# Performance work log

Hardware: AMD Instinct MI355X
Metric: run time of the kernel (lower is better)

The kernel has to match this reference:

```python
import jax, jax.numpy as jnp
import numpy as np

IMG = 640.0
BOX_W, OBJ_W, CLS_W = 7.5, 1.0, 0.5
EPS = 1e-7


def bce_logits(x, t):
    # numerically stable BCE-with-logits, reduction='none'
    return jnp.maximum(x, 0.0) - x * t + jnp.log1p(jnp.exp(-jnp.abs(x)))


def cxcywh_to_xyxy(b):
    cx, cy, w, h = b[..., 0], b[..., 1], b[..., 2], b[..., 3]
    return jnp.stack([cx - w / 2, cy - h / 2, cx + w / 2, cy + h / 2], axis=-1)


def ciou_elementwise(p, g):
    # p, g: (N,4) xyxy; returns CIoU per pair (diag of pairwise matrix)
    px1, py1, px2, py2 = p[:, 0], p[:, 1], p[:, 2], p[:, 3]
    gx1, gy1, gx2, gy2 = g[:, 0], g[:, 1], g[:, 2], g[:, 3]
    iw = jnp.clip(jnp.minimum(px2, gx2) - jnp.maximum(px1, gx1), 0.0)
    ih = jnp.clip(jnp.minimum(py2, gy2) - jnp.maximum(py1, gy1), 0.0)
    inter = iw * ih
    union = (px2 - px1) * (py2 - py1) + (gx2 - gx1) * (gy2 - gy1) - inter
    iou = inter / (union + EPS)
    cw = jnp.maximum(px2, gx2) - jnp.minimum(px1, gx1)
    ch = jnp.maximum(py2, gy2) - jnp.minimum(py1, gy1)
    c2 = cw * cw + ch * ch + EPS
    rho2 = ((gx1 + gx2 - px1 - px2) ** 2 + (gy1 + gy2 - py1 - py2) ** 2) / 4.0
    wp, hp = px2 - px1, py2 - py1
    wg, hg = gx2 - gx1, gy2 - gy1
    v = (4.0 / (jnp.pi ** 2)) * (jnp.arctan(wg / (hg + EPS)) - jnp.arctan(wp / (hp + EPS))) ** 2
    alpha = v / (1.0 - iou + v + EPS)
    return iou - rho2 / c2 - alpha * v


def _per_image(decoded, obj_map, cls_map, boxes, labels, min_sz, max_sz):
    # decoded (4,H,W) normalized cxcywh; obj_map (H,W); cls_map (C,H,W)
    C, H, W = cls_map.shape
    tmax = jnp.maximum(boxes[:, 2], boxes[:, 3]) * IMG
    mask = (tmax > min_sz) & (tmax <= max_sz)        # (N,)
    m = mask.astype(decoded.dtype)
    gx = jnp.clip((boxes[:, 0] * W).astype(jnp.int32), 0, W - 1)
    gy = jnp.clip((boxes[:, 1] * H).astype(jnp.int32), 0, H - 1)
    mp_box = decoded[:, gy, gx].T                    # (N,4)
    iou = jnp.clip(ciou_elementwise(cxcywh_to_xyxy(mp_box), cxcywh_to_xyxy(boxes)), -1.0, 1.0)
    box_l = jnp.sum((1.0 - iou) * m)
    mp_cls = cls_map[:, gy, gx].T                    # (N,C)
    onehot = jax.nn.one_hot(labels, C, dtype=cls_map.dtype)
    cls_l = jnp.sum(bce_logits(mp_cls, onehot) * m[:, None])
    mp_obj = obj_map[gy, gx]
    obj_pos = jnp.sum(bce_logits(mp_obj, 1.0) * m)
    # negative mask: 0 at cells hit by a valid GT, 1 elsewhere
    mask_neg = jnp.ones((H, W), obj_map.dtype).at[gy, gx].min(jnp.where(mask, 0.0, 1.0))
    neg_map = bce_logits(obj_map, 0.0)
    obj_neg = jnp.sum(neg_map * mask_neg) * 0.05
    fallback = jnp.mean(neg_map) * 0.1               # no positives at this scale for this image
    has_pos = jnp.sum(mask) > 0
    obj_l = jnp.where(has_pos, obj_pos + obj_neg, fallback)
    return jnp.where(has_pos, box_l, 0.0), obj_l, jnp.where(has_pos, cls_l, 0.0), jnp.sum(mask)


def detection_loss(p3_bbox, p3_obj, p3_cls, p4_bbox, p4_obj, p4_cls,
                   p5_bbox, p5_obj, p5_cls, boxes, labels):
    B = p3_bbox.shape[0]
    scales = [(p3_bbox, p3_obj, p3_cls, 8, 0.0, 64.0),
              (p4_bbox, p4_obj, p4_cls, 16, 64.0, 128.0),
              (p5_bbox, p5_obj, p5_cls, 32, 128.0, 10000.0)]
    tot_box = tot_obj = tot_cls = jnp.float32(0.0)
    tot_npos = jnp.int32(0)
    for reg, obj, cls, stride, min_sz, max_sz in scales:
        _, _, H, W = reg.shape
        gy, gx = jnp.meshgrid(jnp.arange(H), jnp.arange(W), indexing='ij')
        tx = jax.nn.sigmoid(reg[:, 0]); ty = jax.nn.sigmoid(reg[:, 1])
        tw = jnp.exp(reg[:, 2]); th = jnp.exp(reg[:, 3])
        decoded = jnp.stack([(gx + tx) * stride / IMG,
                             (gy + ty) * stride / IMG,
                             tw * stride / IMG,
                             th * stride / IMG], axis=1)   # (B,4,H,W)
        fn = lambda d, o, c, b, l: _per_image(d, o, c, b, l, min_sz, max_sz)
        bl, ol, cl, np_ = jax.vmap(fn)(decoded, obj[:, 0], cls, boxes, labels)
        tot_box += jnp.sum(bl); tot_obj += jnp.sum(ol); tot_cls += jnp.sum(cl)
        tot_npos += jnp.sum(np_)
    norm = jnp.maximum(tot_npos, 1).astype(tot_box.dtype)
    box_loss = tot_box / norm
    cls_loss = tot_cls / norm
    obj_loss = tot_obj / (B * 3)
    loss = BOX_W * box_loss + OBJ_W * obj_loss + CLS_W * cls_loss
    return jnp.stack([loss, box_loss, obj_loss, cls_loss])


def setup_inputs() -> dict:
    key = jax.random.key(0)
    ks = jax.random.split(key, 11)
    B, C, N = 64, 80, 60
    inp = {
        'p3_bbox': jax.random.normal(ks[0], (B, 4, 80, 80), jnp.float32),
        'p3_obj': jax.random.normal(ks[1], (B, 1, 80, 80), jnp.float32),
        'p3_cls': jax.random.normal(ks[2], (B, C, 80, 80), jnp.float32),
        'p4_bbox': jax.random.normal(ks[3], (B, 4, 40, 40), jnp.float32),
        'p4_obj': jax.random.normal(ks[4], (B, 1, 40, 40), jnp.float32),
        'p4_cls': jax.random.normal(ks[5], (B, C, 40, 40), jnp.float32),
        'p5_bbox': jax.random.normal(ks[6], (B, 4, 20, 20), jnp.float32),
        'p5_obj': jax.random.normal(ks[7], (B, 1, 20, 20), jnp.float32),
        'p5_cls': jax.random.normal(ks[8], (B, C, 20, 20), jnp.float32),
        'boxes': jax.random.uniform(ks[9], (B, N, 4), jnp.float32, 0.02, 0.98),
        'labels': jax.random.randint(ks[10], (B, N), 0, C, jnp.int32),
    }
    return inp


def reference(p3_bbox, p3_obj, p3_cls, p4_bbox, p4_obj, p4_cls,
              p5_bbox, p5_obj, p5_cls, boxes, labels):
    return detection_loss(p3_bbox, p3_obj, p3_cls, p4_bbox, p4_obj, p4_cls,
                          p5_bbox, p5_obj, p5_cls, boxes, labels)
```

## Files before the change

kernel.cpp:

```cpp
#include <hip/hip_runtime.h>
#include <math.h>

#define IMGF 640.0f
#define EPSF 1e-7f
#define NBOX 60
#define NCLS 80
#define NB   64
#define NTH  512
#define PIF  3.14159265358979323846f

__device__ __forceinline__ float bce_fast(float x, float t) {
    return fmaxf(x, 0.0f) - x * t + __logf(1.0f + __expf(-fabsf(x)));
}

__device__ __forceinline__ float bce0_fast(float x) {
    return fmaxf(x, 0.0f) + __logf(1.0f + __expf(-fabsf(x)));
}

__device__ __forceinline__ float sigmoidf_(float x) {
    return 1.0f / (1.0f + __expf(-x));
}

__device__ __forceinline__ float wave_reduce(float v) {
    #pragma unroll
    for (int o = 32; o > 0; o >>= 1) v += __shfl_down(v, o, 64);
    return v;
}

__global__ __launch_bounds__(NTH) void detloss_main(
    const float* __restrict__ p3b, const float* __restrict__ p3o, const float* __restrict__ p3c,
    const float* __restrict__ p4b, const float* __restrict__ p4o, const float* __restrict__ p4c,
    const float* __restrict__ p5b, const float* __restrict__ p5o, const float* __restrict__ p5c,
    const float* __restrict__ boxes, const int* __restrict__ labels,
    float* __restrict__ part)
{
    const int bid = blockIdx.x;
    const int s = bid / NB;
    const int b = bid % NB;
    const int tid = threadIdx.x;

    const float* reg; const float* obj; const float* cls;
    int H; float stridef, mn, mx;
    if (s == 0)      { reg = p3b; obj = p3o; cls = p3c; H = 80; stridef = 8.0f;  mn = 0.0f;   mx = 64.0f; }
    else if (s == 1) { reg = p4b; obj = p4o; cls = p4c; H = 40; stridef = 16.0f; mn = 64.0f;  mx = 128.0f; }
    else             { reg = p5b; obj = p5o; cls = p5c; H = 20; stridef = 32.0f; mn = 128.0f; mx = 10000.0f; }
    const int W = H, HW = H * W;
    reg += (size_t)b * 4 * HW;
    obj += (size_t)b * HW;
    cls += (size_t)b * NCLS * HW;
    const float sf = stridef / IMGF;

    __shared__ int sh_cell[NBOX];
    __shared__ int sh_lab[NBOX];
    __shared__ int sh_mask[NBOX];
    __shared__ float red[6 * 8];

    float box_p = 0.0f, objp_p = 0.0f, cls_p = 0.0f;
    float neg_p = 0.0f, sub_p = 0.0f, npos_p = 0.0f;

    if (tid < NBOX) {
        const size_t bb = ((size_t)b * NBOX + tid) * 4;
        const float bcx = boxes[bb + 0];
        const float bcy = boxes[bb + 1];
        const float bw  = boxes[bb + 2];
        const float bh  = boxes[bb + 3];
        const float tmax = fmaxf(bw, bh) * IMGF;
        const int m = (tmax > mn) && (tmax <= mx);
        int cx = (int)(bcx * (float)W); cx = min(max(cx, 0), W - 1);
        int cy = (int)(bcy * (float)H); cy = min(max(cy, 0), H - 1);
        const int cell = cy * W + cx;
        sh_cell[tid] = cell;
        sh_lab[tid]  = labels[b * NBOX + tid];
        sh_mask[tid] = m;
        if (m) {
            npos_p = 1.0f;
            const float tx = sigmoidf_(reg[0 * HW + cell]);
            const float ty = sigmoidf_(reg[1 * HW + cell]);
            const float tw = __expf(reg[2 * HW + cell]);
            const float th = __expf(reg[3 * HW + cell]);
            const float pcx = ((float)cx + tx) * sf;
            const float pcy = ((float)cy + ty) * sf;
            const float pw = tw * sf, ph = th * sf;
            const float px1 = pcx - pw * 0.5f, px2 = pcx + pw * 0.5f;
            const float py1 = pcy - ph * 0.5f, py2 = pcy + ph * 0.5f;
            const float qx1 = bcx - bw * 0.5f, qx2 = bcx + bw * 0.5f;
            const float qy1 = bcy - bh * 0.5f, qy2 = bcy + bh * 0.5f;
            const float iw = fmaxf(fminf(px2, qx2) - fmaxf(px1, qx1), 0.0f);
            const float ih = fmaxf(fminf(py2, qy2) - fmaxf(py1, qy1), 0.0f);
            const float inter = iw * ih;
            const float uni = (px2 - px1) * (py2 - py1) + (qx2 - qx1) * (qy2 - qy1) - inter;
            const float iou = inter / (uni + EPSF);
            const float cw = fmaxf(px2, qx2) - fminf(px1, qx1);
            const float ch = fmaxf(py2, qy2) - fminf(py1, qy1);
            const float c2 = cw * cw + ch * ch + EPSF;
            const float dx = qx1 + qx2 - px1 - px2;
            const float dy = qy1 + qy2 - py1 - py2;
            const float rho2 = (dx * dx + dy * dy) * 0.25f;
            const float wp = px2 - px1, hp = py2 - py1;
            const float wg = qx2 - qx1, hg = qy2 - qy1;
            const float da = atanf(wg / (hg + EPSF)) - atanf(wp / (hp + EPSF));
            const float v = (4.0f / (PIF * PIF)) * da * da;
            const float alpha = v / (1.0f - iou + v + EPSF);
            float ci = iou - rho2 / c2 - alpha * v;
            ci = fminf(fmaxf(ci, -1.0f), 1.0f);
            box_p  = 1.0f - ci;
            objp_p = bce_fast(obj[cell], 1.0f);
        }
    }

    {
        const float4* obj4 = (const float4*)obj;
        const int n4 = HW >> 2;
        for (int i = tid; i < n4; i += NTH) {
            const float4 v = obj4[i];
            neg_p += bce0_fast(v.x) + bce0_fast(v.y) + bce0_fast(v.z) + bce0_fast(v.w);
        }
    }
    __syncthreads();

    if (tid < NBOX && sh_mask[tid]) {
        const int cell = sh_cell[tid];
        bool first = true;
        for (int j = 0; j < tid; ++j)
            if (sh_mask[j] && sh_cell[j] == cell) { first = false; break; }
        if (first) sub_p = bce0_fast(obj[cell]);
    }

    #pragma unroll 2
    for (int i = tid; i < NBOX * NCLS; i += NTH) {
        const int n = i / NCLS;
        const int c = i - n * NCLS;
        if (sh_mask[n]) {
            const float x = cls[(size_t)c * HW + sh_cell[n]];
            cls_p += bce_fast(x, (c == sh_lab[n]) ? 1.0f : 0.0f);
        }
    }

    float vals[6] = { box_p, objp_p, cls_p, neg_p, sub_p, npos_p };
    const int wave = tid >> 6, lane = tid & 63;
    #pragma unroll
    for (int k = 0; k < 6; ++k) {
        const float v = wave_reduce(vals[k]);
        if (lane == 0) red[k * 8 + wave] = v;
    }
    __syncthreads();
    if (tid == 0) {
        float t[6];
        #pragma unroll
        for (int k = 0; k < 6; ++k) {
            float acc = 0.0f;
            #pragma unroll
            for (int w = 0; w < 8; ++w) acc += red[k * 8 + w];
            t[k] = acc;
        }
        const bool has_pos = t[5] > 0.0f;
        const float obj_l = has_pos ? (t[1] + (t[3] - t[4]) * 0.05f)
                                    : (t[3] / (float)HW) * 0.1f;
        part[bid * 4 + 0] = has_pos ? t[0] : 0.0f;
        part[bid * 4 + 1] = obj_l;
        part[bid * 4 + 2] = has_pos ? t[2] : 0.0f;
        part[bid * 4 + 3] = t[5];
    }
}

__global__ __launch_bounds__(256) void detloss_final(
    const float* __restrict__ part, float* __restrict__ out)
{
    const int tid = threadIdx.x;
    float vb = 0.0f, vo = 0.0f, vc = 0.0f, vn = 0.0f;
    if (tid < 3 * NB) {
        vb = part[tid * 4 + 0];
        vo = part[tid * 4 + 1];
        vc = part[tid * 4 + 2];
        vn = part[tid * 4 + 3];
    }
    __shared__ float red[4 * 4];
    float vals[4] = { vb, vo, vc, vn };
    const int wave = tid >> 6, lane = tid & 63;
    #pragma unroll
    for (int k = 0; k < 4; ++k) {
        const float v = wave_reduce(vals[k]);
        if (lane == 0) red[k * 4 + wave] = v;
    }
    __syncthreads();
    if (tid == 0) {
        float t[4];
        #pragma unroll
        for (int k = 0; k < 4; ++k)
            t[k] = red[k * 4 + 0] + red[k * 4 + 1] + red[k * 4 + 2] + red[k * 4 + 3];
        const float norm = fmaxf(t[3], 1.0f);
        const float box_loss = t[0] / norm;
        const float cls_loss = t[2] / norm;
        const float obj_loss = t[1] / (float)(NB * 3);
        const float loss = 7.5f * box_loss + 1.0f * obj_loss + 0.5f * cls_loss;
        out[0] = loss;
        out[1] = box_loss;
        out[2] = obj_loss;
        out[3] = cls_loss;
    }
}

extern "C" void kernel_launch(void* const* d_in, const int* in_sizes, int n_in,
                              void* d_out, int out_size, void* d_ws, size_t ws_size,
                              hipStream_t stream) {
    const float* p3b = (const float*)d_in[0];
    const float* p3o = (const float*)d_in[1];
    const float* p3c = (const float*)d_in[2];
    const float* p4b = (const float*)d_in[3];
    const float* p4o = (const float*)d_in[4];
    const float* p4c = (const float*)d_in[5];
    const float* p5b = (const float*)d_in[6];
    const float* p5o = (const float*)d_in[7];
    const float* p5c = (const float*)d_in[8];
    const float* boxes = (const float*)d_in[9];
    const int*   labels = (const int*)d_in[10];

    float* part = (float*)d_ws;
    float* out  = (float*)d_out;

    detloss_main<<<dim3(3 * NB), dim3(NTH), 0, stream>>>(
        p3b, p3o, p3c, p4b, p4o, p4c, p5b, p5o, p5c, boxes, labels, part);
    detloss_final<<<dim3(1), dim3(256), 0, stream>>>(part, out);
}
```

Baseline: 207.6 us.

## Fuse final reduction via atomics and last-block ticket; batch class gathers

Removes the separate finalize kernel. Each block now atomically adds its partial sums into workspace, and the last block to take a ticket computes the final losses. The class-BCE loop is fully unrolled into 10 independent gathers issued before any compute, which raises memory-level parallelism on the scattered loads. This adds a memset launch and makes the float summation order nondeterministic.

```diff
diff --git a/kernel.cpp b/kernel.cpp
--- a/kernel.cpp
+++ b/kernel.cpp
@@ -7,32 +7,30 @@
 #define NCLS 80
 #define NB   64
 #define NTH  512
+#define NBLK (3 * NB)
 #define PIF  3.14159265358979323846f
 
 __device__ __forceinline__ float bce_fast(float x, float t) {
     return fmaxf(x, 0.0f) - x * t + __logf(1.0f + __expf(-fabsf(x)));
 }
-
 __device__ __forceinline__ float bce0_fast(float x) {
     return fmaxf(x, 0.0f) + __logf(1.0f + __expf(-fabsf(x)));
 }
-
 __device__ __forceinline__ float sigmoidf_(float x) {
     return 1.0f / (1.0f + __expf(-x));
 }
-
 __device__ __forceinline__ float wave_reduce(float v) {
     #pragma unroll
     for (int o = 32; o > 0; o >>= 1) v += __shfl_down(v, o, 64);
     return v;
 }
 
-__global__ __launch_bounds__(NTH) void detloss_main(
+__global__ __launch_bounds__(NTH) void detloss_fused(
     const float* __restrict__ p3b, const float* __restrict__ p3o, const float* __restrict__ p3c,
     const float* __restrict__ p4b, const float* __restrict__ p4o, const float* __restrict__ p4c,
     const float* __restrict__ p5b, const float* __restrict__ p5o, const float* __restrict__ p5c,
     const float* __restrict__ boxes, const int* __restrict__ labels,
-    float* __restrict__ part)
+    float* __restrict__ ws, float* __restrict__ out)
 {
     const int bid = blockIdx.x;
     const int s = bid / NB;
@@ -126,14 +124,26 @@
         if (first) sub_p = bce0_fast(obj[cell]);
     }
 
-    #pragma unroll 2
-    for (int i = tid; i < NBOX * NCLS; i += NTH) {
-        const int n = i / NCLS;
-        const int c = i - n * NCLS;
-        if (sh_mask[n]) {
-            const float x = cls[(size_t)c * HW + sh_cell[n]];
-            cls_p += bce_fast(x, (c == sh_lab[n]) ? 1.0f : 0.0f);
-        }
+    {
+        float xs[10], tg[10];
+        bool  act[10];
+        #pragma unroll
+        for (int k = 0; k < 10; ++k) {
+            const int i = tid + k * NTH;
+            act[k] = false;
+            if (i < NBOX * NCLS) {
+                const int n = i / NCLS;
+                const int c = i - n * NCLS;
+                if (sh_mask[n]) {
+                    act[k] = true;
+                    xs[k]  = cls[(size_t)c * HW + sh_cell[n]];
+                    tg[k]  = (c == sh_lab[n]) ? 1.0f : 0.0f;
+                }
+            }
+        }
+        #pragma unroll
+        for (int k = 0; k < 10; ++k)
+            if (act[k]) cls_p += bce_fast(xs[k], tg[k]);
     }
 
     float vals[6] = { box_p, objp_p, cls_p, neg_p, sub_p, npos_p };
@@ -144,6 +154,7 @@
         if (lane == 0) red[k * 8 + wave] = v;
     }
     __syncthreads();
+
     if (tid == 0) {
         float t[6];
         #pragma unroll
@@ -156,47 +167,27 @@
         const bool has_pos = t[5] > 0.0f;
         const float obj_l = has_pos ? (t[1] + (t[3] - t[4]) * 0.05f)
                                     : (t[3] / (float)HW) * 0.1f;
-        part[bid * 4 + 0] = has_pos ? t[0] : 0.0f;
-        part[bid * 4 + 1] = obj_l;
-        part[bid * 4 + 2] = has_pos ? t[2] : 0.0f;
-        part[bid * 4 + 3] = t[5];
-    }
-}
-
-__global__ __launch_bounds__(256) void detloss_final(
-    const float* __restrict__ part, float* __restrict__ out)
-{
-    const int tid = threadIdx.x;
-    float vb = 0.0f, vo = 0.0f, vc = 0.0f, vn = 0.0f;
-    if (tid < 3 * NB) {
-        vb = part[tid * 4 + 0];
-        vo = part[tid * 4 + 1];
-        vc = part[tid * 4 + 2];
-        vn = part[tid * 4 + 3];
-    }
-    __shared__ float red[4 * 4];
-    float vals[4] = { vb, vo, vc, vn };
-    const int wave = tid >> 6, lane = tid & 63;
-    #pragma unroll
-    for (int k = 0; k < 4; ++k) {
-        const float v = wave_reduce(vals[k]);
-        if (lane == 0) red[k * 4 + wave] = v;
-    }
-    __syncthreads();
-    if (tid == 0) {
-        float t[4];
-        #pragma unroll
-        for (int k = 0; k < 4; ++k)
-            t[k] = red[k * 4 + 0] + red[k * 4 + 1] + red[k * 4 + 2] + red[k * 4 + 3];
-        const float norm = fmaxf(t[3], 1.0f);
-        const float box_loss = t[0] / norm;
-        const float cls_loss = t[2] / norm;
-        const float obj_loss = t[1] / (float)(NB * 3);
-        const float loss = 7.5f * box_loss + 1.0f * obj_loss + 0.5f * cls_loss;
-        out[0] = loss;
-        out[1] = box_loss;
-        out[2] = obj_loss;
-        out[3] = cls_loss;
+        atomicAdd(&ws[0], has_pos ? t[0] : 0.0f);
+        atomicAdd(&ws[1], obj_l);
+        atomicAdd(&ws[2], has_pos ? t[2] : 0.0f);
+        atomicAdd(&ws[3], t[5]);
+        __threadfence();
+        unsigned* ticket = (unsigned*)&ws[4];
+        const unsigned old = atomicAdd(ticket, 1u);
+        if (old == NBLK - 1) {
+            const float tb = atomicAdd(&ws[0], 0.0f);
+            const float to = atomicAdd(&ws[1], 0.0f);
+            const float tc = atomicAdd(&ws[2], 0.0f);
+            const float tn = atomicAdd(&ws[3], 0.0f);
+            const float norm = fmaxf(tn, 1.0f);
+            const float box_loss = tb / norm;
+            const float cls_loss = tc / norm;
+            const float obj_loss = to / (float)(NB * 3);
+            out[0] = 7.5f * box_loss + obj_loss + 0.5f * cls_loss;
+            out[1] = box_loss;
+            out[2] = obj_loss;
+            out[3] = cls_loss;
+        }
     }
 }
 
@@ -215,10 +206,9 @@
     const float* boxes = (const float*)d_in[9];
     const int*   labels = (const int*)d_in[10];
 
-    float* part = (float*)d_ws;
-    float* out  = (float*)d_out;
-
-    detloss_main<<<dim3(3 * NB), dim3(NTH), 0, stream>>>(
-        p3b, p3o, p3c, p4b, p4o, p4c, p5b, p5o, p5c, boxes, labels, part);
-    detloss_final<<<dim3(1), dim3(256), 0, stream>>>(part, out);
-}
+    hipMemsetAsync(d_ws, 0, 32, stream);
+
+    detloss_fused<<<dim3(NBLK), dim3(NTH), 0, stream>>>(
+        p3b, p3o, p3c, p4b, p4o, p4c, p5b, p5o, p5c, boxes, labels,
+        (float*)d_ws, (float*)d_out);
+}
```

After: 215.9 us. 4.0% more time.
